# Kernel optimization log

Hardware: AMD Instinct MI355X
Metric: run time of the kernel (lower is better)

The kernel has to match this reference:

```python
import jax, jax.numpy as jnp
import numpy as np

N_STEPS = 6
LN_EPS = 1e-5

def _lin(x, w, b):
    # torch Linear: y = x @ W^T + b, w: [out, in]
    return jnp.matmul(x, w.T) + b

def _gelu(x):
    return jax.nn.gelu(x, approximate=False)

def setup_inputs() -> dict:
    key = jax.random.key(0)
    B, T, D, C, V, MS = 8, 1024, 512, 512, 32000, 1024
    ks = jax.random.split(key, 16)
    w = lambda k, shape: (jax.random.normal(k, shape, jnp.float32) * 0.02)
    return {
        "tokens": jax.random.randint(ks[0], (B, T), 0, V),
        "c_states": jax.random.normal(ks[1], (4, C), jnp.float32),
        "embed_w": w(ks[2], (V, D)),
        "pos_w": w(ks[3], (MS, D)),
        "cn_w1": w(ks[4], (2 * D, 4 * D)), "cn_b1": jnp.zeros((2 * D,), jnp.float32),
        "cn_w2": w(ks[5], (D, 2 * D)), "cn_b2": jnp.zeros((D,), jnp.float32),
        "ent_w1": w(ks[6], (64, D)), "ent_b1": jnp.zeros((64,), jnp.float32),
        "ent_w2": w(ks[7], (1, 64)), "ent_b2": jnp.zeros((1,), jnp.float32),
        "ctc_w1": w(ks[8], (2 * D, C)), "ctc_b1": jnp.zeros((2 * D,), jnp.float32),
        "ctc_w2": w(ks[9], (D, 2 * D)), "ctc_b2": jnp.zeros((D,), jnp.float32),
        "base_temp": jnp.asarray(2.0, jnp.float32),
        "ln_g": jnp.ones((D,), jnp.float32), "ln_b": jnp.zeros((D,), jnp.float32),
        "head_w": w(ks[10], (V, D)),
    }

def reference(tokens, c_states, embed_w, pos_w, cn_w1, cn_b1, cn_w2, cn_b2,
              ent_w1, ent_b1, ent_w2, ent_b2, ctc_w1, ctc_b1, ctc_w2, ctc_b2,
              base_temp, ln_g, ln_b, head_w):
    B, T = tokens.shape
    x = embed_w[tokens] + pos_w[:T][None, :, :]          # [B,T,D]
    c_pooled = c_states.mean(axis=0)                      # [C]
    c_constraint = _lin(_gelu(_lin(c_pooled, ctc_w1, ctc_b1)), ctc_w2, ctc_b2)  # [D]
    c_exp = jnp.broadcast_to(c_constraint, (B, T, c_constraint.shape[0]))
    sp_temp = jax.nn.softplus(base_temp)
    for step in range(N_STEPS):
        temp = sp_temp * (1.0 - step / N_STEPS * 0.8)
        left = jnp.roll(x, 1, axis=1)
        right = jnp.roll(x, -1, axis=1)
        ci = jnp.concatenate([x, left, right, c_exp], axis=-1)  # [B,T,4D]
        constraint = _lin(_gelu(_lin(ci, cn_w1, cn_b1)), cn_w2, cn_b2)  # [B,T,D]
        entropy = _lin(_gelu(_lin(x, ent_w1, ent_b1)), ent_w2, ent_b2)[..., 0]  # [B,T]
        cw = jax.nn.softmax(-entropy / temp, axis=-1)            # softmax over T
        x = x + constraint * cw[..., None] * 0.3
    mu = x.mean(axis=-1, keepdims=True)
    var = ((x - mu) ** 2).mean(axis=-1, keepdims=True)
    xn = (x - mu) * jax.lax.rsqrt(var + LN_EPS) * ln_g + ln_b
    return jnp.matmul(xn, head_w.T)                        # [B,T,V]
```

## Files before the change

### kernel.cpp

```cpp
#include <hip/hip_runtime.h>
#include <hip/hip_bf16.h>

typedef __hip_bfloat16 bf16_t;
typedef __bf16 bf16x8_t __attribute__((ext_vector_type(8)));
typedef float f32x4_t __attribute__((ext_vector_type(4)));

#define OFF_X     ((size_t)0)
#define OFF_XB    ((size_t)16777216)
#define OFF_H1    ((size_t)25165824)
#define OFF_XN    ((size_t)41943040)
#define OFF_HEADB ((size_t)50331648)
#define OFF_W1B   ((size_t)83099648)
#define OFF_W2B   ((size_t)86245376)
#define OFF_EW1   ((size_t)87293952)
#define OFF_ENT   ((size_t)87359488)
#define OFF_CW    ((size_t)87392256)
#define OFF_HC    ((size_t)87425024)
#define OFF_CC    ((size_t)87429120)
#define OFF_B1    ((size_t)87431168)

__device__ __forceinline__ float gelu_f(float v) {
    return 0.5f * v * (1.0f + erff(v * 0.7071067811865475f));
}

__device__ __forceinline__ void load_lds16(const bf16_t* g, bf16_t* l) {
    __builtin_amdgcn_global_load_lds(
        (const __attribute__((address_space(1))) void*)g,
        (__attribute__((address_space(3))) void*)l, 16, 0, 0);
}

#define BAR()    __builtin_amdgcn_s_barrier()
#define SCHED0() __builtin_amdgcn_sched_barrier(0)
#define LGKM0()  asm volatile("s_waitcnt lgkmcnt(0)" ::: "memory")
#define WAITV0() asm volatile("s_waitcnt vmcnt(0)" ::: "memory")
#define WAITV2() asm volatile("s_waitcnt vmcnt(2)" ::: "memory")
#define WAITV4() asm volatile("s_waitcnt vmcnt(4)" ::: "memory")

__global__ void prep1_kernel(const float* __restrict__ cs, const float* __restrict__ w1,
                             const float* __restrict__ b1, float* __restrict__ hc) {
    int o = blockIdx.x * 256 + threadIdx.x;
    const float* wr = w1 + (size_t)o * 512;
    float acc = 0.f;
    for (int k = 0; k < 512; k += 4) {
        float4 w4 = *(const float4*)(wr + k);
        float4 a = *(const float4*)(cs + k);
        float4 b = *(const float4*)(cs + 512 + k);
        float4 c = *(const float4*)(cs + 1024 + k);
        float4 d = *(const float4*)(cs + 1536 + k);
        acc += w4.x * (a.x + b.x + c.x + d.x) * 0.25f;
        acc += w4.y * (a.y + b.y + c.y + d.y) * 0.25f;
        acc += w4.z * (a.z + b.z + c.z + d.z) * 0.25f;
        acc += w4.w * (a.w + b.w + c.w + d.w) * 0.25f;
    }
    hc[o] = gelu_f(acc + b1[o]);
}

__global__ void prep2_kernel(const float* __restrict__ hc, const float* __restrict__ w2,
                             const float* __restrict__ b2, float* __restrict__ cc) {
    int o = blockIdx.x * 256 + threadIdx.x;
    const float* wr = w2 + (size_t)o * 1024;
    float acc = 0.f;
    for (int k = 0; k < 1024; ++k) acc += wr[k] * hc[k];
    cc[o] = acc + b2[o];
}

__global__ void prep3_kernel(const float* __restrict__ cc, const float* __restrict__ cn_w1,
                             const float* __restrict__ cn_b1, float* __restrict__ bias1) {
    int o = blockIdx.x * 256 + threadIdx.x;
    const float* wr = cn_w1 + (size_t)o * 2048 + 1536;
    float acc = 0.f;
    for (int k = 0; k < 512; ++k) acc += wr[k] * cc[k];
    bias1[o] = acc + cn_b1[o];
}

__global__ void embed_kernel(const int* __restrict__ tokens, const float* __restrict__ ew,
                             const float* __restrict__ pw, float* __restrict__ x,
                             bf16_t* __restrict__ xb) {
    int idx = blockIdx.x * 256 + threadIdx.x;
    int d4 = idx & 127;
    int bt = idx >> 7;
    int t = bt & 1023;
    int tok = tokens[bt];
    float4 e = ((const float4*)(ew + (size_t)tok * 512))[d4];
    float4 p = ((const float4*)(pw + (size_t)t * 512))[d4];
    float4 o = make_float4(e.x + p.x, e.y + p.y, e.z + p.z, e.w + p.w);
    ((float4*)x)[idx] = o;
    __hip_bfloat162 p0, p1;
    p0.x = __float2bfloat16(o.x); p0.y = __float2bfloat16(o.y);
    p1.x = __float2bfloat16(o.z); p1.y = __float2bfloat16(o.w);
    ((__hip_bfloat162*)xb)[idx * 2]     = p0;
    ((__hip_bfloat162*)xb)[idx * 2 + 1] = p1;
}

__global__ void cvt_kernel(const float* __restrict__ src, bf16_t* __restrict__ dst) {
    int idx = blockIdx.x * 256 + threadIdx.x;
    float4 v = ((const float4*)src)[idx];
    __hip_bfloat162 p0, p1;
    p0.x = __float2bfloat16(v.x); p0.y = __float2bfloat16(v.y);
    p1.x = __float2bfloat16(v.z); p1.y = __float2bfloat16(v.w);
    ((__hip_bfloat162*)dst)[idx * 2]     = p0;
    ((__hip_bfloat162*)dst)[idx * 2 + 1] = p1;
}

__global__ void cvt_w1_kernel(const float* __restrict__ w1, bf16_t* __restrict__ dst) {
    int idx = blockIdx.x * 256 + threadIdx.x;
    int k4 = idx % 384;
    int o = idx / 384;
    float4 v = ((const float4*)(w1 + (size_t)o * 2048))[k4];
    __hip_bfloat162 p0, p1;
    p0.x = __float2bfloat16(v.x); p0.y = __float2bfloat16(v.y);
    p1.x = __float2bfloat16(v.z); p1.y = __float2bfloat16(v.w);
    ((__hip_bfloat162*)dst)[idx * 2]     = p0;
    ((__hip_bfloat162*)dst)[idx * 2 + 1] = p1;
}

__global__ __launch_bounds__(256) void entropy_mfma(
        const bf16_t* __restrict__ xb, const bf16_t* __restrict__ w1b,
        const float* __restrict__ b1, const float* __restrict__ w2,
        const float* __restrict__ b2, float* __restrict__ ent) {
    int wave = threadIdx.x >> 6, lane = threadIdx.x & 63;
    int lr = lane & 15, kq = lane >> 4;
    int tok0 = (blockIdx.x * 4 + wave) * 16;
    f32x4_t acc[4] = {};
    const bf16_t* xr = xb + (size_t)(tok0 + lr) * 512 + kq * 8;
    const bf16_t* wr = w1b + (size_t)lr * 512 + kq * 8;
    #pragma unroll 4
    for (int k0 = 0; k0 < 512; k0 += 32) {
        bf16x8_t a = *(const bf16x8_t*)(xr + k0);
        #pragma unroll
        for (int j = 0; j < 4; ++j) {
            bf16x8_t bb = *(const bf16x8_t*)(wr + (size_t)j * 16 * 512 + k0);
            acc[j] = __builtin_amdgcn_mfma_f32_16x16x32_bf16(a, bb, acc[j], 0, 0, 0);
        }
    }
    float p[4];
    #pragma unroll
    for (int r = 0; r < 4; ++r) {
        float s = 0.f;
        #pragma unroll
        for (int j = 0; j < 4; ++j) {
            int n = j * 16 + lr;
            s += gelu_f(acc[j][r] + b1[n]) * w2[n];
        }
        #pragma unroll
        for (int o = 1; o < 16; o <<= 1) s += __shfl_xor(s, o);
        p[r] = s;
    }
    if (lr == 0) {
        float bb = b2[0];
        #pragma unroll
        for (int r = 0; r < 4; ++r) ent[tok0 + kq * 4 + r] = p[r] + bb;
    }
}

__global__ void softmax_kernel(const float* __restrict__ ent, const float* __restrict__ btp,
                               float stepf, float* __restrict__ cw) {
    __shared__ float red[16];
    __shared__ float bc[2];
    int b = blockIdx.x, t = threadIdx.x;
    float bt = btp[0];
    float sp = (bt > 20.0f) ? bt : log1pf(expf(bt));
    float inv = -1.0f / (sp * stepf);
    float v = ent[b * 1024 + t] * inv;
    float m = v;
    #pragma unroll
    for (int o = 32; o; o >>= 1) m = fmaxf(m, __shfl_xor(m, o));
    if ((t & 63) == 0) red[t >> 6] = m;
    __syncthreads();
    if (t < 64) {
        float mm = (t < 16) ? red[t] : -3.4e38f;
        #pragma unroll
        for (int o = 32; o; o >>= 1) mm = fmaxf(mm, __shfl_xor(mm, o));
        if (t == 0) bc[0] = mm;
    }
    __syncthreads();
    float e = expf(v - bc[0]);
    float s = e;
    #pragma unroll
    for (int o = 32; o; o >>= 1) s += __shfl_xor(s, o);
    if ((t & 63) == 0) red[t >> 6] = s;
    __syncthreads();
    if (t < 64) {
        float ss = (t < 16) ? red[t] : 0.f;
        #pragma unroll
        for (int o = 32; o; o >>= 1) ss += __shfl_xor(ss, o);
        if (t == 0) bc[1] = ss;
    }
    __syncthreads();
    cw[b * 1024 + t] = e / bc[1];
}

__global__ void ln_kernel(const float* __restrict__ x, const float* __restrict__ g,
                          const float* __restrict__ b, bf16_t* __restrict__ xn) {
    int token = blockIdx.x * 4 + (threadIdx.x >> 6);
    int l = threadIdx.x & 63;
    const float* xr = x + (size_t)token * 512;
    float4 v0 = ((const float4*)xr)[l * 2];
    float4 v1 = ((const float4*)xr)[l * 2 + 1];
    float s = v0.x + v0.y + v0.z + v0.w + v1.x + v1.y + v1.z + v1.w;
    float ss = v0.x * v0.x + v0.y * v0.y + v0.z * v0.z + v0.w * v0.w
             + v1.x * v1.x + v1.y * v1.y + v1.z * v1.z + v1.w * v1.w;
    #pragma unroll
    for (int o = 32; o; o >>= 1) { s += __shfl_xor(s, o); ss += __shfl_xor(ss, o); }
    float mu = s * (1.0f / 512.0f);
    float var = ss * (1.0f / 512.0f) - mu * mu;
    float rs = rsqrtf(var + 1e-5f);
    float4 g0 = ((const float4*)g)[l * 2], g1 = ((const float4*)g)[l * 2 + 1];
    float4 b0 = ((const float4*)b)[l * 2], b1 = ((const float4*)b)[l * 2 + 1];
    bf16_t* op = xn + (size_t)token * 512 + l * 8;
    op[0] = __float2bfloat16((v0.x - mu) * rs * g0.x + b0.x);
    op[1] = __float2bfloat16((v0.y - mu) * rs * g0.y + b0.y);
    op[2] = __float2bfloat16((v0.z - mu) * rs * g0.z + b0.z);
    op[3] = __float2bfloat16((v0.w - mu) * rs * g0.w + b0.w);
    op[4] = __float2bfloat16((v1.x - mu) * rs * g1.x + b1.x);
    op[5] = __float2bfloat16((v1.y - mu) * rs * g1.y + b1.y);
    op[6] = __float2bfloat16((v1.z - mu) * rs * g1.z + b1.z);
    op[7] = __float2bfloat16((v1.w - mu) * rs * g1.w + b1.w);
}

template <int MODE, int ROLL, int BN>
__global__ __launch_bounds__(512, 2) void gemm8p(
    const bf16_t* __restrict__ A, int lda,
    const bf16_t* __restrict__ B, int ldb, int K, int NMT,
    const float* __restrict__ bias,
    bf16_t* __restrict__ out_bf, int ldc,
    const float* __restrict__ cw, float* __restrict__ x,
    float* __restrict__ out_f)
{
    constexpr int JJ = BN / 64;
    __shared__ __align__(16) bf16_t As[2][256 * 64];
    __shared__ __align__(16) bf16_t Bs[2][BN * 64];

    const int NT = K >> 6;
    const int nwg = gridDim.x;
    const int id0 = blockIdx.x;
    const int id = (id0 & 7) * (nwg >> 3) + (id0 >> 3);
    const int m0 = (id % NMT) * 256;
    const int n0 = (id / NMT) * BN;

    const int tid = threadIdx.x;
    const int wave = tid >> 6, lane = tid & 63;
    const int wm = (wave >> 2) * 128;
    const int wn = (wave & 3) * (BN / 4);
    const int lr = lane & 15, kq = lane >> 4;

    const int swz0 = (kq)     ^ (lr & 7);
    const int swz1 = (4 + kq) ^ (lr & 7);
    const int eoff0 = lr * 64 + swz0 * 8;
    const int eoff1 = lr * 64 + swz1 * 8;

    const int u0row = tid >> 3;
    const int u1row = 64 + (tid >> 3);
    const int usl   = tid & 7;
    const int c0 = ((usl ^ (u0row & 7)) * 8);
    const int c1 = ((usl ^ (u1row & 7)) * 8);

    f32x4_t acc[8][JJ] = {};
    bf16x8_t bfr[JJ][2];

    auto stageA = [&](int ktile, int c, int half) {
        const int kbase = ktile << 6;
        const int r0 = m0 + half * 128 + u0row;
        const int r1 = m0 + half * 128 + u1row;
        const bf16_t *g0, *g1;
        if (ROLL) {
            const int seg = kbase >> 9;
            const int kk2 = kbase & 511;
            const int sh = (seg == 0) ? 0 : ((seg == 1) ? 1023 : 1);
            const int s0 = (r0 & ~1023) | (((r0 & 1023) + sh) & 1023);
            const int s1 = (r1 & ~1023) | (((r1 & 1023) + sh) & 1023);
            g0 = A + (size_t)s0 * 512 + kk2 + c0;
            g1 = A + (size_t)s1 * 512 + kk2 + c1;
        } else {
            g0 = A + (size_t)r0 * lda + kbase + c0;
            g1 = A + (size_t)r1 * lda + kbase + c1;
        }
        bf16_t* l = &As[c][half * 128 * 64];
        load_lds16(g0, l + tid * 8);
        load_lds16(g1, l + (tid + 512) * 8);
    };
    auto stageB = [&](int ktile, int c, int half) {
        const int kbase = ktile << 6;
        const int r0 = n0 + half * 128 + u0row;
        const int r1 = n0 + half * 128 + u1row;
        const bf16_t* g0 = B + (size_t)r0 * ldb + kbase + c0;
        const bf16_t* g1 = B + (size_t)r1 * ldb + kbase + c1;
        bf16_t* l = &Bs[c][half * 128 * 64];
        load_lds16(g0, l + tid * 8);
        load_lds16(g1, l + (tid + 512) * 8);
    };

    stageA(0, 0, 0); stageA(0, 0, 1);
    stageB(0, 0, 0); if (BN == 256) stageB(0, 0, 1);
    stageB(1, 1, 0); if (BN == 256) stageB(1, 1, 1);
    if (BN == 256) { WAITV4(); } else { WAITV2(); }
    BAR();

    int cur = 0;
    for (int t = 0; t < NT; ++t) {
        #pragma unroll
        for (int p = 0; p < 4; ++p) {
            bf16x8_t af0k0, af0k1, af1k0, af1k1;
            {
                const int r0 = (wm + 32 * p + lr) * 64;
                const int r1 = (wm + 32 * p + 16 + lr) * 64;
                af0k0 = *(const bf16x8_t*)&As[cur][r0 - lr * 64 + eoff0];
                af0k1 = *(const bf16x8_t*)&As[cur][r0 - lr * 64 + eoff1];
                af1k0 = *(const bf16x8_t*)&As[cur][r1 - lr * 64 + eoff0];
                af1k1 = *(const bf16x8_t*)&As[cur][r1 - lr * 64 + eoff1];
            }
            if (p == 0) {
                #pragma unroll
                for (int j = 0; j < JJ; ++j) {
                    const int rb = (wn + 16 * j) * 64;
                    bfr[j][0] = *(const bf16x8_t*)&Bs[cur][rb + eoff0];
                    bfr[j][1] = *(const bf16x8_t*)&Bs[cur][rb + eoff1];
                }
            }
            if (p == 0 && t + 1 < NT) stageA(t + 1, cur ^ 1, 0);
            if (p == 1 && t + 1 < NT) stageA(t + 1, cur ^ 1, 1);
            if (p == 2 && t + 2 < NT) stageB(t + 2, cur, 0);
            if (p == 3 && BN == 256 && t + 2 < NT) stageB(t + 2, cur, 1);

            BAR();
            LGKM0();
            SCHED0();
            __builtin_amdgcn_s_setprio(1);
            #pragma unroll
            for (int j = 0; j < JJ; ++j) {
                acc[2*p][j]   = __builtin_amdgcn_mfma_f32_16x16x32_bf16(af0k0, bfr[j][0], acc[2*p][j],   0, 0, 0);
                acc[2*p+1][j] = __builtin_amdgcn_mfma_f32_16x16x32_bf16(af1k0, bfr[j][0], acc[2*p+1][j], 0, 0, 0);
            }
            #pragma unroll
            for (int j = 0; j < JJ; ++j) {
                acc[2*p][j]   = __builtin_amdgcn_mfma_f32_16x16x32_bf16(af0k1, bfr[j][1], acc[2*p][j],   0, 0, 0);
                acc[2*p+1][j] = __builtin_amdgcn_mfma_f32_16x16x32_bf16(af1k1, bfr[j][1], acc[2*p+1][j], 0, 0, 0);
            }
            __builtin_amdgcn_s_setprio(0);
            SCHED0();
            if (p == 3) {
                if (t + 2 < NT) { if (BN == 256) { WAITV4(); } else { WAITV2(); } }
                else           { WAITV0(); }
            }
            BAR();
        }
        cur ^= 1;
    }

    #pragma unroll
    for (int i = 0; i < 8; ++i) {
        const int rbase = m0 + wm + i * 16 + kq * 4;
        #pragma unroll
        for (int j = 0; j < JJ; ++j) {
            const int gcol = n0 + wn + j * 16 + lr;
            #pragma unroll
            for (int r = 0; r < 4; ++r) {
                const size_t grow = (size_t)(rbase + r);
                float v = acc[i][j][r];
                if (MODE == 0) {
                    v = gelu_f(v + bias[gcol]);
                    out_bf[grow * ldc + gcol] = __float2bfloat16(v);
                } else if (MODE == 1) {
                    v += bias[gcol];
                    float nv = x[grow * ldc + gcol] + v * cw[grow] * 0.3f;
                    x[grow * ldc + gcol] = nv;
                    out_bf[grow * ldc + gcol] = __float2bfloat16(nv);
                } else {
                    out_f[grow * ldc + gcol] = v;
                }
            }
        }
    }
}

extern "C" void kernel_launch(void* const* d_in, const int* in_sizes, int n_in,
                              void* d_out, int out_size, void* d_ws, size_t ws_size,
                              hipStream_t stream) {
    const int*   tokens   = (const int*)d_in[0];
    const float* c_states = (const float*)d_in[1];
    const float* embed_w  = (const float*)d_in[2];
    const float* pos_w    = (const float*)d_in[3];
    const float* cn_w1    = (const float*)d_in[4];
    const float* cn_b1    = (const float*)d_in[5];
    const float* cn_w2    = (const float*)d_in[6];
    const float* cn_b2    = (const float*)d_in[7];
    const float* ent_w1   = (const float*)d_in[8];
    const float* ent_b1   = (const float*)d_in[9];
    const float* ent_w2   = (const float*)d_in[10];
    const float* ent_b2   = (const float*)d_in[11];
    const float* ctc_w1   = (const float*)d_in[12];
    const float* ctc_b1   = (const float*)d_in[13];
    const float* ctc_w2   = (const float*)d_in[14];
    const float* ctc_b2   = (const float*)d_in[15];
    const float* base_temp= (const float*)d_in[16];
    const float* ln_g     = (const float*)d_in[17];
    const float* ln_b     = (const float*)d_in[18];
    const float* head_w   = (const float*)d_in[19];
    float* out = (float*)d_out;

    char* ws = (char*)d_ws;
    float*  x     = (float*)(ws + OFF_X);
    bf16_t* xb    = (bf16_t*)(ws + OFF_XB);
    bf16_t* h1    = (bf16_t*)(ws + OFF_H1);
    bf16_t* xn    = (bf16_t*)(ws + OFF_XN);
    bf16_t* headb = (bf16_t*)(ws + OFF_HEADB);
    bf16_t* w1b   = (bf16_t*)(ws + OFF_W1B);
    bf16_t* w2b   = (bf16_t*)(ws + OFF_W2B);
    bf16_t* ew1b  = (bf16_t*)(ws + OFF_EW1);
    float*  ent   = (float*)(ws + OFF_ENT);
    float*  cw    = (float*)(ws + OFF_CW);
    float*  hc    = (float*)(ws + OFF_HC);
    float*  cc    = (float*)(ws + OFF_CC);
    float*  bias1 = (float*)(ws + OFF_B1);

    cvt_w1_kernel<<<1536, 256, 0, stream>>>(cn_w1, w1b);
    cvt_kernel<<<512, 256, 0, stream>>>(cn_w2, w2b);
    cvt_kernel<<<32, 256, 0, stream>>>(ent_w1, ew1b);
    prep1_kernel<<<4, 256, 0, stream>>>(c_states, ctc_w1, ctc_b1, hc);
    prep2_kernel<<<2, 256, 0, stream>>>(hc, ctc_w2, ctc_b2, cc);
    prep3_kernel<<<4, 256, 0, stream>>>(cc, cn_w1, cn_b1, bias1);
    embed_kernel<<<4096, 256, 0, stream>>>(tokens, embed_w, pos_w, x, xb);

    for (int step = 0; step < 6; ++step) {
        float stepf = 1.0f - ((float)step / 6.0f) * 0.8f;
        entropy_mfma<<<128, 256, 0, stream>>>(xb, ew1b, ent_b1, ent_w2, ent_b2, ent);
        softmax_kernel<<<8, 1024, 0, stream>>>(ent, base_temp, stepf, cw);
        gemm8p<0, 1, 128><<<256, 512, 0, stream>>>(xb, 512, w1b, 1536, 1536, 32,
                                                   bias1, h1, 1024, nullptr, nullptr, nullptr);
        gemm8p<1, 0, 128><<<128, 512, 0, stream>>>(h1, 1024, w2b, 1024, 1024, 32,
                                                   cn_b2, xb, 512, cw, x, nullptr);
    }

    cvt_kernel<<<16000, 256, 0, stream>>>(head_w, headb);
    ln_kernel<<<2048, 256, 0, stream>>>(x, ln_g, ln_b, xn);
    gemm8p<2, 0, 256><<<4000, 512, 0, stream>>>(xn, 512, headb, 512, 512, 32,
                                                nullptr, nullptr, 32000, nullptr, nullptr, out);
}
```

Before: 1.205 ms.

## Fuse entropy MLP with softmax and merge weight conversion launches

Merges the entropy MLP and the per-batch softmax into one kernel: each 1024-thread block computes its batch's 1024 entropies into shared memory, then runs the softmax, which removes a launch and the global round trip for the entropy values. The three weight conversion kernels are also merged into one launch. In exchange, the entropy work now runs on only 8 blocks instead of 128, so each wave does four times as much serial MFMA work and far fewer CUs participate.

```diff
diff --git a/kernel.cpp b/kernel.cpp
--- a/kernel.cpp
+++ b/kernel.cpp
@@ -13,7 +13,6 @@
 #define OFF_W1B   ((size_t)83099648)
 #define OFF_W2B   ((size_t)86245376)
 #define OFF_EW1   ((size_t)87293952)
-#define OFF_ENT   ((size_t)87359488)
 #define OFF_CW    ((size_t)87392256)
 #define OFF_HC    ((size_t)87425024)
 #define OFF_CC    ((size_t)87429120)
@@ -92,102 +91,121 @@
     ((__hip_bfloat162*)xb)[idx * 2 + 1] = p1;
 }
 
+__device__ __forceinline__ void cvt_store(const float4 v, __hip_bfloat162* dst) {
+    __hip_bfloat162 p0, p1;
+    p0.x = __float2bfloat16(v.x); p0.y = __float2bfloat16(v.y);
+    p1.x = __float2bfloat16(v.z); p1.y = __float2bfloat16(v.w);
+    dst[0] = p0; dst[1] = p1;
+}
+
 __global__ void cvt_kernel(const float* __restrict__ src, bf16_t* __restrict__ dst) {
     int idx = blockIdx.x * 256 + threadIdx.x;
     float4 v = ((const float4*)src)[idx];
-    __hip_bfloat162 p0, p1;
-    p0.x = __float2bfloat16(v.x); p0.y = __float2bfloat16(v.y);
-    p1.x = __float2bfloat16(v.z); p1.y = __float2bfloat16(v.w);
-    ((__hip_bfloat162*)dst)[idx * 2]     = p0;
-    ((__hip_bfloat162*)dst)[idx * 2 + 1] = p1;
-}
-
-__global__ void cvt_w1_kernel(const float* __restrict__ w1, bf16_t* __restrict__ dst) {
-    int idx = blockIdx.x * 256 + threadIdx.x;
-    int k4 = idx % 384;
-    int o = idx / 384;
-    float4 v = ((const float4*)(w1 + (size_t)o * 2048))[k4];
-    __hip_bfloat162 p0, p1;
-    p0.x = __float2bfloat16(v.x); p0.y = __float2bfloat16(v.y);
-    p1.x = __float2bfloat16(v.z); p1.y = __float2bfloat16(v.w);
-    ((__hip_bfloat162*)dst)[idx * 2]     = p0;
-    ((__hip_bfloat162*)dst)[idx * 2 + 1] = p1;
-}
-
-__global__ __launch_bounds__(256) void entropy_mfma(
+    cvt_store(v, (__hip_bfloat162*)dst + idx * 2);
+}
+
+__global__ void cvt3_kernel(const float* __restrict__ cn_w1, const float* __restrict__ cn_w2,
+                            const float* __restrict__ ent_w1,
+                            bf16_t* __restrict__ w1b, bf16_t* __restrict__ w2b,
+                            bf16_t* __restrict__ ew1b) {
+    int bid = blockIdx.x;
+    if (bid < 1536) {
+        int idx = bid * 256 + threadIdx.x;
+        int k4 = idx % 384;
+        int o = idx / 384;
+        float4 v = ((const float4*)(cn_w1 + (size_t)o * 2048))[k4];
+        cvt_store(v, (__hip_bfloat162*)w1b + idx * 2);
+    } else if (bid < 2048) {
+        int idx = (bid - 1536) * 256 + threadIdx.x;
+        float4 v = ((const float4*)cn_w2)[idx];
+        cvt_store(v, (__hip_bfloat162*)w2b + idx * 2);
+    } else {
+        int idx = (bid - 2048) * 256 + threadIdx.x;
+        float4 v = ((const float4*)ent_w1)[idx];
+        cvt_store(v, (__hip_bfloat162*)ew1b + idx * 2);
+    }
+}
+
+__global__ __launch_bounds__(1024) void entsm_kernel(
         const bf16_t* __restrict__ xb, const bf16_t* __restrict__ w1b,
         const float* __restrict__ b1, const float* __restrict__ w2,
-        const float* __restrict__ b2, float* __restrict__ ent) {
-    int wave = threadIdx.x >> 6, lane = threadIdx.x & 63;
-    int lr = lane & 15, kq = lane >> 4;
-    int tok0 = (blockIdx.x * 4 + wave) * 16;
-    f32x4_t acc[4] = {};
-    const bf16_t* xr = xb + (size_t)(tok0 + lr) * 512 + kq * 8;
-    const bf16_t* wr = w1b + (size_t)lr * 512 + kq * 8;
-    #pragma unroll 4
-    for (int k0 = 0; k0 < 512; k0 += 32) {
-        bf16x8_t a = *(const bf16x8_t*)(xr + k0);
-        #pragma unroll
-        for (int j = 0; j < 4; ++j) {
-            bf16x8_t bb = *(const bf16x8_t*)(wr + (size_t)j * 16 * 512 + k0);
-            acc[j] = __builtin_amdgcn_mfma_f32_16x16x32_bf16(a, bb, acc[j], 0, 0, 0);
-        }
-    }
-    float p[4];
-    #pragma unroll
-    for (int r = 0; r < 4; ++r) {
-        float s = 0.f;
-        #pragma unroll
-        for (int j = 0; j < 4; ++j) {
-            int n = j * 16 + lr;
-            s += gelu_f(acc[j][r] + b1[n]) * w2[n];
-        }
-        #pragma unroll
-        for (int o = 1; o < 16; o <<= 1) s += __shfl_xor(s, o);
-        p[r] = s;
-    }
-    if (lr == 0) {
-        float bb = b2[0];
-        #pragma unroll
-        for (int r = 0; r < 4; ++r) ent[tok0 + kq * 4 + r] = p[r] + bb;
-    }
-}
-
-__global__ void softmax_kernel(const float* __restrict__ ent, const float* __restrict__ btp,
-                               float stepf, float* __restrict__ cw) {
+        const float* __restrict__ b2, const float* __restrict__ btp,
+        float stepf, float* __restrict__ cw) {
+    __shared__ float ents[1024];
     __shared__ float red[16];
     __shared__ float bc[2];
-    int b = blockIdx.x, t = threadIdx.x;
+    const int b = blockIdx.x;
+    const int tid = threadIdx.x;
+    const int wave = tid >> 6, lane = tid & 63;
+    const int lr = lane & 15, kq = lane >> 4;
+
+    const bf16_t* wr = w1b + (size_t)lr * 512 + kq * 8;
+    const float eb2 = b2[0];
+    #pragma unroll
+    for (int g = 0; g < 4; ++g) {
+        const int trel = wave * 64 + g * 16;
+        const int tok0 = b * 1024 + trel;
+        f32x4_t acc[4] = {};
+        const bf16_t* xr = xb + (size_t)(tok0 + lr) * 512 + kq * 8;
+        #pragma unroll 4
+        for (int k0 = 0; k0 < 512; k0 += 32) {
+            bf16x8_t a = *(const bf16x8_t*)(xr + k0);
+            #pragma unroll
+            for (int j = 0; j < 4; ++j) {
+                bf16x8_t bb = *(const bf16x8_t*)(wr + (size_t)j * 16 * 512 + k0);
+                acc[j] = __builtin_amdgcn_mfma_f32_16x16x32_bf16(a, bb, acc[j], 0, 0, 0);
+            }
+        }
+        float p[4];
+        #pragma unroll
+        for (int r = 0; r < 4; ++r) {
+            float s = 0.f;
+            #pragma unroll
+            for (int j = 0; j < 4; ++j) {
+                int n = j * 16 + lr;
+                s += gelu_f(acc[j][r] + b1[n]) * w2[n];
+            }
+            #pragma unroll
+            for (int o = 1; o < 16; o <<= 1) s += __shfl_xor(s, o);
+            p[r] = s;
+        }
+        if (lr == 0) {
+            #pragma unroll
+            for (int r = 0; r < 4; ++r) ents[trel + kq * 4 + r] = p[r] + eb2;
+        }
+    }
+    __syncthreads();
+
     float bt = btp[0];
     float sp = (bt > 20.0f) ? bt : log1pf(expf(bt));
     float inv = -1.0f / (sp * stepf);
-    float v = ent[b * 1024 + t] * inv;
+    float v = ents[tid] * inv;
     float m = v;
     #pragma unroll
     for (int o = 32; o; o >>= 1) m = fmaxf(m, __shfl_xor(m, o));
-    if ((t & 63) == 0) red[t >> 6] = m;
+    if (lane == 0) red[wave] = m;
     __syncthreads();
-    if (t < 64) {
-        float mm = (t < 16) ? red[t] : -3.4e38f;
+    if (tid < 64) {
+        float mm = (tid < 16) ? red[tid] : -3.4e38f;
         #pragma unroll
         for (int o = 32; o; o >>= 1) mm = fmaxf(mm, __shfl_xor(mm, o));
-        if (t == 0) bc[0] = mm;
+        if (tid == 0) bc[0] = mm;
     }
     __syncthreads();
     float e = expf(v - bc[0]);
     float s = e;
     #pragma unroll
     for (int o = 32; o; o >>= 1) s += __shfl_xor(s, o);
-    if ((t & 63) == 0) red[t >> 6] = s;
+    if (lane == 0) red[wave] = s;
     __syncthreads();
-    if (t < 64) {
-        float ss = (t < 16) ? red[t] : 0.f;
+    if (tid < 64) {
+        float ss = (tid < 16) ? red[tid] : 0.f;
         #pragma unroll
         for (int o = 32; o; o >>= 1) ss += __shfl_xor(ss, o);
-        if (t == 0) bc[1] = ss;
+        if (tid == 0) bc[1] = ss;
     }
     __syncthreads();
-    cw[b * 1024 + t] = e / bc[1];
+    cw[b * 1024 + tid] = e / bc[1];
 }
 
 __global__ void ln_kernel(const float* __restrict__ x, const float* __restrict__ g,
@@ -407,15 +425,12 @@
     bf16_t* w1b   = (bf16_t*)(ws + OFF_W1B);
     bf16_t* w2b   = (bf16_t*)(ws + OFF_W2B);
     bf16_t* ew1b  = (bf16_t*)(ws + OFF_EW1);
-    float*  ent   = (float*)(ws + OFF_ENT);
     float*  cw    = (float*)(ws + OFF_CW);
     float*  hc    = (float*)(ws + OFF_HC);
     float*  cc    = (float*)(ws + OFF_CC);
     float*  bias1 = (float*)(ws + OFF_B1);
 
-    cvt_w1_kernel<<<1536, 256, 0, stream>>>(cn_w1, w1b);
-    cvt_kernel<<<512, 256, 0, stream>>>(cn_w2, w2b);
-    cvt_kernel<<<32, 256, 0, stream>>>(ent_w1, ew1b);
+    cvt3_kernel<<<2080, 256, 0, stream>>>(cn_w1, cn_w2, ent_w1, w1b, w2b, ew1b);
     prep1_kernel<<<4, 256, 0, stream>>>(c_states, ctc_w1, ctc_b1, hc);
     prep2_kernel<<<2, 256, 0, stream>>>(hc, ctc_w2, ctc_b2, cc);
     prep3_kernel<<<4, 256, 0, stream>>>(cc, cn_w1, cn_b1, bias1);
@@ -423,8 +438,8 @@
 
     for (int step = 0; step < 6; ++step) {
         float stepf = 1.0f - ((float)step / 6.0f) * 0.8f;
-        entropy_mfma<<<128, 256, 0, stream>>>(xb, ew1b, ent_b1, ent_w2, ent_b2, ent);
-        softmax_kernel<<<8, 1024, 0, stream>>>(ent, base_temp, stepf, cw);
+        entsm_kernel<<<8, 1024, 0, stream>>>(xb, ew1b, ent_b1, ent_w2, ent_b2,
+                                             base_temp, stepf, cw);
         gemm8p<0, 1, 128><<<256, 512, 0, stream>>>(xb, 512, w1b, 1536, 1536, 32,
                                                    bias1, h1, 1024, nullptr, nullptr, nullptr);
         gemm8p<1, 0, 128><<<128, 512, 0, stream>>>(h1, 1024, w2b, 1024, 1024, 32,
```

After: 1.963 ms. 62.9% more time.
